# Kernel tuning notes

Measured on AMD Instinct MI355X. Metric: run time of the kernel, lower is better.

The kernel has to match this reference:

```python
import jax, jax.numpy as jnp
import numpy as np
import math

B, L, D = 8, 2048, 256
NUM_TYPES = 1
T_MAX = 200.0
SIGMA = 1.0


def setup_inputs() -> dict:
    key = jax.random.key(0)
    ks = jax.random.split(key, 12)
    event_type = jnp.ones((B, L), dtype=jnp.int64 if jax.config.jax_enable_x64 else jnp.int32)
    t = jax.random.uniform(ks[0], (B, L), dtype=jnp.float32) * T_MAX
    event_time = jnp.sort(t, axis=-1)
    s = 1.0 / math.sqrt(D)
    emb_weight = jax.random.normal(ks[1], (NUM_TYPES + 1, D), jnp.float32)
    emb_weight = emb_weight.at[0].set(0.0)  # padding_idx=0
    gate_w = jax.random.normal(ks[2], (2, D), jnp.float32) * s
    gate_b = jnp.zeros((2,), jnp.float32)
    ker_w = jax.random.normal(ks[3], (1, D), jnp.float32) * s
    ker_b = jnp.zeros((1,), jnp.float32)
    ln_gamma = jnp.ones((D,), jnp.float32)
    ln_beta = jnp.zeros((D,), jnp.float32)
    gen_input_w = jax.random.normal(ks[4], (D, D), jnp.float32) * s
    gen_noise_w = jax.random.normal(ks[5], (D, D), jnp.float32) * s
    gen_out_w = jax.random.normal(ks[6], (1, D), jnp.float32) * s
    gen_out_b = jnp.zeros((1,), jnp.float32)
    noise = jax.random.uniform(ks[7], (B, L, D), jnp.float32)  # torch.rand noise in Generator
    return dict(event_type=event_type, event_time=event_time, emb_weight=emb_weight,
                gate_w=gate_w, gate_b=gate_b, ker_w=ker_w, ker_b=ker_b,
                ln_gamma=ln_gamma, ln_beta=ln_beta, gen_input_w=gen_input_w,
                gen_noise_w=gen_noise_w, gen_out_w=gen_out_w, gen_out_b=gen_out_b,
                noise=noise)


def _softplus_beta(x, beta):
    return jax.nn.softplus(beta * x) / beta


def reference(event_type, event_time, emb_weight, gate_w, gate_b, ker_w, ker_b,
              ln_gamma, ln_beta, gen_input_w, gen_noise_w, gen_out_w, gen_out_b, noise):
    d_model = emb_weight.shape[-1]
    # ---- temporal positional encoding (this is `embedding`) ----
    pos_vec = jnp.power(10000.0, 2.0 * jnp.arange(d_model, dtype=jnp.float32) / d_model)
    t = event_time[:, :, None] / pos_vec                      # [B,L,D]
    idx = jnp.arange(d_model)
    temp_enc = jnp.where(idx % 2 == 0, jnp.sin(t), jnp.cos(t))
    # ---- type embedding ----
    te = emb_weight[event_type] * math.sqrt(d_model)          # [B,L,D]
    # ---- pairwise |t_i - t_j| ; xt[b,i,j]=t_i, xt_bar[b,i,j]=t_j ----
    dt = jnp.abs(event_time[:, :, None] - event_time[:, None, :])  # [B,L,L]
    # ---- squared exponential kernel: params depend only on row i (xd[b,i,j]=te[b,i]) ----
    ls = _softplus_beta(te @ ker_w.T + ker_b, 0.2)[..., 0]    # [B,L]
    scores_k = (SIGMA ** 2) * jnp.exp(-(dt ** 2) / (ls[:, :, None] ** 2))
    # ---- sigmoid gate ----
    p = jax.nn.sigmoid(te @ gate_w.T + gate_b)                # [B,L,2]
    l = p[..., 0][:, :, None]
    s = p[..., 1][:, :, None]
    gate = 1.0 + 0.5 * jnp.tanh((dt / T_MAX - l) / s)
    scores = scores_k * gate                                  # [B,L,L]
    # ---- causal mask: strictly-upper-triangle -> -1e10, then softmax ----
    causal = jnp.tril(jnp.ones((event_time.shape[1], event_time.shape[1]), jnp.bool_))
    scores = jnp.where(causal[None], scores, -1e10)
    attn = jax.nn.softmax(scores, axis=-1)
    # ---- hidden = attn @ temp_enc, layernorm ----
    hidden = jnp.einsum('bij,bjd->bid', attn, temp_enc)
    mu = hidden.mean(-1, keepdims=True)
    var = hidden.var(-1, keepdims=True)
    hidden = (hidden - mu) / jnp.sqrt(var + 1e-6) * ln_gamma + ln_beta
    # ---- Generator (dropout in eval = identity) ----
    h = jax.nn.relu(noise @ gen_noise_w.T + hidden @ gen_input_w.T)
    out = jax.nn.softplus(h @ gen_out_w.T + gen_out_b)[..., 0]  # [B,L]
    return out
```

## Files before the change

### kernel.cpp

```cpp
#include <hip/hip_runtime.h>
#include <hip/hip_bf16.h>

#define BD 8
#define LD 2048
#define DD 256

typedef unsigned short ushort_t;
typedef __attribute__((ext_vector_type(8))) short short8;
typedef __attribute__((ext_vector_type(4))) float floatx4;

__device__ __forceinline__ ushort_t f2bfu(float x) {
  __hip_bfloat16 h = __float2bfloat16(x);
  return *reinterpret_cast<ushort_t*>(&h);
}

__device__ __forceinline__ void dma16(const ushort_t* g, ushort_t* l) {
  __builtin_amdgcn_global_load_lds(
      (const __attribute__((address_space(1))) unsigned int*)g,
      (__attribute__((address_space(3))) unsigned int*)l,
      16, 0, 0);
}

#define WAIT_VM0  0x0F70
#define WAIT_VM8  0x0F78
#define WAIT_VM10 0x0F7A
#define WAIT_LGKM 0xC07F

__device__ __forceinline__ float sin_acc(float a) {
  float k = rintf(a * 0.15915494f);
  float r = __builtin_fmaf(-k, 6.2831855f, a);
  r = __builtin_fmaf(-k, -1.7484555e-7f, r);
  return __sinf(r);
}
__device__ __forceinline__ float cos_acc(float a) {
  float k = rintf(a * 0.15915494f);
  float r = __builtin_fmaf(-k, 6.2831855f, a);
  r = __builtin_fmaf(-k, -1.7484555e-7f, r);
  return __cosf(r);
}

__global__ __launch_bounds__(256) void k_prep(
    const int* __restrict__ etype, const float* __restrict__ etime,
    const float* __restrict__ embw, const float* __restrict__ gatew,
    const float* __restrict__ gateb, const float* __restrict__ kerw,
    const float* __restrict__ kerb, const float* __restrict__ noise,
    const float* __restrict__ wn, const float* __restrict__ wi,
    ushort_t* __restrict__ enc_bf, ushort_t* __restrict__ noise_bf,
    ushort_t* __restrict__ wcat, float* __restrict__ ptable)
{
  const int bk = blockIdx.x;
  const int tid = threadIdx.x;
  if (bk < 4224) {
    int idx = bk * 256 + tid;
    if (idx < 1048576) {
      float4 f = ((const float4*)noise)[idx];
      ushort4 u;
      u.x = f2bfu(f.x); u.y = f2bfu(f.y); u.z = f2bfu(f.z); u.w = f2bfu(f.w);
      *(ushort4*)(noise_bf + (size_t)idx * 4) = u;
    } else {
      int p = idx - 1048576;
      int c = p >> 7;
      int k = (p & 127) * 4;
      const float* src = (k < 256) ? (wn + c * 256 + k) : (wi + c * 256 + (k - 256));
      float4 f = *(const float4*)src;
      ushort4 u;
      u.x = f2bfu(f.x); u.y = f2bfu(f.y); u.z = f2bfu(f.z); u.w = f2bfu(f.w);
      *(ushort4*)(wcat + (((size_t)(c >> 4) * 16 + (k >> 5)) * 512)
                       + (c & 15) * 32 + (k & 31)) = u;
    }
  } else if (bk < 4736) {
    int ebk = bk - 4224;
    __shared__ float ts[32];
    if (tid < 32) ts[tid] = etime[(ebk >> 6) * LD + (ebk & 63) * 32 + tid];
    __syncthreads();
    uint4* dst = (uint4*)(enc_bf + (size_t)ebk * 8192);
    const int jb = (tid & 3) * 8;
    #pragma unroll
    for (int jblk = 0; jblk < 4; ++jblk) {
      int d = jblk * 64 + (tid >> 2);
      float freq = __expf(-0.07195578416f * (float)d);
      unsigned int pk[4];
      #pragma unroll
      for (int p = 0; p < 4; ++p) {
        float a0 = ts[jb + 2 * p] * freq;
        float a1 = ts[jb + 2 * p + 1] * freq;
        float v0 = (d & 1) ? cos_acc(a0) : sin_acc(a0);
        float v1 = (d & 1) ? cos_acc(a1) : sin_acc(a1);
        pk[p] = (unsigned int)f2bfu(v0) | ((unsigned int)f2bfu(v1) << 16);
      }
      dst[jblk * 256 + tid] = make_uint4(pk[0], pk[1], pk[2], pk[3]);
    }
  } else {
    __shared__ float red[4][3];
    int lane = tid & 63, wvi = tid >> 6;
    for (int ty = 0; ty < 2; ++ty) {
      float te = embw[ty * DD + tid] * 16.0f;
      float p1 = te * kerw[tid];
      float p2 = te * gatew[tid];
      float p3 = te * gatew[DD + tid];
      #pragma unroll
      for (int off = 32; off > 0; off >>= 1) {
        p1 += __shfl_xor(p1, off);
        p2 += __shfl_xor(p2, off);
        p3 += __shfl_xor(p3, off);
      }
      if (lane == 0) { red[wvi][0] = p1; red[wvi][1] = p2; red[wvi][2] = p3; }
      __syncthreads();
      if (tid == 0) {
        float s1 = red[0][0] + red[1][0] + red[2][0] + red[3][0] + kerb[0];
        float s2 = red[0][1] + red[1][1] + red[2][1] + red[3][1] + gateb[0];
        float s3 = red[0][2] + red[1][2] + red[2][2] + red[3][2] + gateb[1];
        float z = 0.2f * s1;
        float sp = (z > 15.0f) ? z : log1pf(__expf(z));
        float ls = 5.0f * sp;
        ptable[ty * 4 + 0] = 1.0f / (ls * ls);
        ptable[ty * 4 + 1] = 1.0f / (1.0f + __expf(-s2));
        float s = 1.0f / (1.0f + __expf(-s3));
        ptable[ty * 4 + 2] = 1.0f / s;
      }
      __syncthreads();
    }
  }
}

__global__ __launch_bounds__(128) void k_attn(
    const ushort_t* __restrict__ enc_bf, const float* __restrict__ etime,
    const int* __restrict__ etype, const float* __restrict__ ptable,
    const float* __restrict__ gamma, const float* __restrict__ beta,
    ushort_t* __restrict__ hidden_bf)
{
  __shared__ __align__(16) ushort_t stage[2][2][4096];
  const int tid = threadIdx.x;
  const int lane = tid & 63, wv = tid >> 6;
  const int bk = blockIdx.x;
  const int b = bk & 7;
  const int tl = 127 - (bk >> 3);
  const int base = b * LD;
  const int m = lane & 15, kg = lane >> 4;
  const int i = tl * 16 + m;
  const float ti = etime[base + i];
  const int ty = etype[base + i];
  const float il = ptable[ty * 4 + 0];
  const float ll = ptable[ty * 4 + 1];
  const float is2 = 2.0f * ptable[ty * 4 + 2];
  floatx4 acc[16];
  #pragma unroll
  for (int nt = 0; nt < 16; ++nt) acc[nt] = (floatx4){0.f, 0.f, 0.f, 0.f};
  const int nch = tl / 2 + 1;
  const int myn = (nch > wv) ? ((nch - wv + 1) >> 1) : 0;
  const ushort_t* __restrict__ encC = enc_bf + (size_t)(b * 64) * 8192;
  const int boff = m * 32 + kg * 8;
  ushort_t* bufA = &stage[wv][0][0];
  ushort_t* bufB = &stage[wv][1][0];

  if (myn > 0) {
    const int c0 = wv;
    float4 ta = *(const float4*)(etime + base + c0 * 32 + kg * 8);
    float4 tc = *(const float4*)(etime + base + c0 * 32 + kg * 8 + 4);
    {
      const ushort_t* g = encC + (size_t)c0 * 8192 + lane * 8;
      #pragma unroll
      for (int q = 0; q < 8; ++q) dma16(g + q * 512, bufA + q * 512);
      #pragma unroll
      for (int q = 0; q < 8; ++q) dma16(g + (q + 8) * 512, bufB + q * 512);
    }
    float tj[8] = {ta.x, ta.y, ta.z, ta.w, tc.x, tc.y, tc.z, tc.w};
    short8 af;
    {
      const int j0 = c0 * 32 + kg * 8;
      #pragma unroll
      for (int v = 0; v < 8; ++v) {
        float dt = ti - tj[v];
        float sk = __expf(-dt * dt * il);
        float rg = __builtin_amdgcn_rcpf(__expf((dt * 0.005f - ll) * is2) + 1.0f);
        float w = __expf(sk * (1.5f - rg));
        w = (j0 + v <= i) ? w : 0.0f;
        af[v] = (short)f2bfu(w);
      }
    }
    for (int idx = 0; idx < myn; ++idx) {
      const int ch = wv + 2 * idx;
      const bool more = (idx + 1 < myn);
      const int cn = more ? (ch + 2) : wv;
      __builtin_amdgcn_s_waitcnt(WAIT_VM8);
      #pragma unroll
      for (int q = 0; q < 8; ++q) {
        short8 bf = *(const short8*)(bufA + q * 512 + boff);
        acc[q] = __builtin_amdgcn_mfma_f32_16x16x32_bf16(af, bf, acc[q], 0, 0, 0);
      }
      float4 na = *(const float4*)(etime + base + cn * 32 + kg * 8);
      float4 nc = *(const float4*)(etime + base + cn * 32 + kg * 8 + 4);
      __builtin_amdgcn_s_waitcnt(WAIT_LGKM);
      {
        const ushort_t* g = encC + (size_t)cn * 8192 + lane * 8;
        #pragma unroll
        for (int q = 0; q < 8; ++q) dma16(g + q * 512, bufA + q * 512);
      }
      __builtin_amdgcn_s_waitcnt(WAIT_VM10);
      #pragma unroll
      for (int q = 0; q < 8; ++q) {
        short8 bf = *(const short8*)(bufB + q * 512 + boff);
        acc[8 + q] = __builtin_amdgcn_mfma_f32_16x16x32_bf16(af, bf, acc[8 + q], 0, 0, 0);
      }
      __builtin_amdgcn_s_waitcnt(WAIT_LGKM);
      {
        const ushort_t* g = encC + (size_t)cn * 8192 + lane * 8;
        #pragma unroll
        for (int q = 0; q < 8; ++q) dma16(g + (q + 8) * 512, bufB + q * 512);
      }
      if (more) {
        float ntj[8] = {na.x, na.y, na.z, na.w, nc.x, nc.y, nc.z, nc.w};
        const int j0 = cn * 32 + kg * 8;
        #pragma unroll
        for (int v = 0; v < 8; ++v) {
          float dt = ti - ntj[v];
          float sk = __expf(-dt * dt * il);
          float rg = __builtin_amdgcn_rcpf(__expf((dt * 0.005f - ll) * is2) + 1.0f);
          float w = __expf(sk * (1.5f - rg));
          w = (j0 + v <= i) ? w : 0.0f;
          af[v] = (short)f2bfu(w);
        }
      }
    }
  }
  __syncthreads();
  floatx4* reg = (floatx4*)&stage[0][0][0];
  if (wv == 1) {
    #pragma unroll
    for (int nt = 0; nt < 16; ++nt) reg[nt * 64 + lane] = acc[nt];
  }
  __syncthreads();
  if (wv == 0) {
    #pragma unroll
    for (int nt = 0; nt < 16; ++nt) acc[nt] += reg[nt * 64 + lane];
    float gl[16], cl[16];
    #pragma unroll
    for (int nt = 0; nt < 16; ++nt) { gl[nt] = gamma[nt * 16 + m]; cl[nt] = beta[nt * 16 + m]; }
    const int q = lane >> 4;
    #pragma unroll
    for (int r = 0; r < 4; ++r) {
      float h[16];
      float sm = 0.0f, sq = 0.0f;
      #pragma unroll
      for (int nt = 0; nt < 16; ++nt) {
        h[nt] = acc[nt][r];
        sm += h[nt]; sq += h[nt] * h[nt];
      }
      #pragma unroll
      for (int off = 1; off < 16; off <<= 1) {
        sm += __shfl_xor(sm, off);
        sq += __shfl_xor(sq, off);
      }
      float mean = sm * (1.0f / 256.0f);
      float var = sq * (1.0f / 256.0f) - mean * mean;
      float rstd = rsqrtf(var + 1e-6f);
      const int row = q * 4 + r;
      ushort_t* dst = hidden_bf + ((size_t)(base + tl * 16 + row)) * DD + m;
      #pragma unroll
      for (int nt = 0; nt < 16; ++nt)
        dst[nt * 16] = f2bfu((h[nt] - mean) * rstd * gl[nt] + cl[nt]);
    }
  }
}

__global__ __launch_bounds__(256) void k_gen(
    const ushort_t* __restrict__ noise_bf, const ushort_t* __restrict__ hidden_bf,
    const ushort_t* __restrict__ wcat, const float* __restrict__ wout,
    const float* __restrict__ bout, float* __restrict__ out)
{
  __shared__ float pbuf[4][2][16];
  const int tid = threadIdx.x;
  const int lane = tid & 63, wv = tid >> 6;
  const int m = lane & 15, kg = lane >> 4;
  const int r0 = blockIdx.x * 32 + m;
  const ushort_t* __restrict__ an0 = noise_bf + (size_t)r0 * DD;
  const ushort_t* __restrict__ an1 = noise_bf + (size_t)(r0 + 16) * DD;
  const ushort_t* __restrict__ ah0 = hidden_bf + (size_t)r0 * DD;
  const ushort_t* __restrict__ ah1 = hidden_bf + (size_t)(r0 + 16) * DD;
  floatx4 acc[2][4];
  #pragma unroll
  for (int t = 0; t < 2; ++t)
    #pragma unroll
    for (int n = 0; n < 4; ++n) acc[t][n] = (floatx4){0.f, 0.f, 0.f, 0.f};
  const int slot = m * 32 + kg * 8;
  #pragma unroll
  for (int ks = 0; ks < 16; ++ks) {
    const int koff = (ks & 7) * 32 + kg * 8;
    short8 a0 = *(const short8*)(((ks < 8) ? an0 : ah0) + koff);
    short8 a1 = *(const short8*)(((ks < 8) ? an1 : ah1) + koff);
    #pragma unroll
    for (int n = 0; n < 4; ++n) {
      const ushort_t* bp = wcat + ((size_t)(wv * 4 + n) * 16 + ks) * 512 + slot;
      short8 bf = *(const short8*)bp;
      acc[0][n] = __builtin_amdgcn_mfma_f32_16x16x32_bf16(a0, bf, acc[0][n], 0, 0, 0);
      acc[1][n] = __builtin_amdgcn_mfma_f32_16x16x32_bf16(a1, bf, acc[1][n], 0, 0, 0);
    }
  }
  float wo_l[4];
  #pragma unroll
  for (int n = 0; n < 4; ++n) wo_l[n] = wout[(wv * 4 + n) * 16 + m];
  #pragma unroll
  for (int t = 0; t < 2; ++t) {
    #pragma unroll
    for (int r4 = 0; r4 < 4; ++r4) {
      float p = 0.0f;
      #pragma unroll
      for (int n = 0; n < 4; ++n) p += fmaxf(acc[t][n][r4], 0.0f) * wo_l[n];
      #pragma unroll
      for (int off = 1; off < 16; off <<= 1) p += __shfl_xor(p, off);
      if (m == 0) pbuf[wv][t][kg * 4 + r4] = p;
    }
  }
  __syncthreads();
  if (tid < 32) {
    int t = tid >> 4, rr = tid & 15;
    float x = pbuf[0][t][rr] + pbuf[1][t][rr] + pbuf[2][t][rr] + pbuf[3][t][rr] + bout[0];
    float sp = (x > 15.0f) ? x : log1pf(__expf(x));
    out[blockIdx.x * 32 + t * 16 + rr] = sp;
  }
}

extern "C" void kernel_launch(void* const* d_in, const int* in_sizes, int n_in,
                              void* d_out, int out_size, void* d_ws, size_t ws_size,
                              hipStream_t stream) {
  const int*   etype = (const int*)d_in[0];
  const float* etime = (const float*)d_in[1];
  const float* embw  = (const float*)d_in[2];
  const float* gatew = (const float*)d_in[3];
  const float* gateb = (const float*)d_in[4];
  const float* kerw  = (const float*)d_in[5];
  const float* kerb  = (const float*)d_in[6];
  const float* gamma = (const float*)d_in[7];
  const float* beta  = (const float*)d_in[8];
  const float* wi    = (const float*)d_in[9];
  const float* wn    = (const float*)d_in[10];
  const float* wo    = (const float*)d_in[11];
  const float* bo    = (const float*)d_in[12];
  const float* noise = (const float*)d_in[13];
  float* out = (float*)d_out;

  char* w8 = (char*)d_ws;
  float* ptable       = (float*)(w8);
  ushort_t* enc_bf    = (ushort_t*)(w8 + 262144);
  ushort_t* hidden_bf = (ushort_t*)(w8 + 262144 + 8388608);
  ushort_t* noise_bf  = (ushort_t*)(w8 + 262144 + 2 * 8388608);
  ushort_t* wcat      = (ushort_t*)(w8 + 262144 + 3 * 8388608);

  k_prep<<<4737, 256, 0, stream>>>(etype, etime, embw, gatew, gateb, kerw, kerb,
                                   noise, wn, wi, enc_bf, noise_bf, wcat, ptable);
  k_attn<<<1024, 128, 0, stream>>>(enc_bf, etime, etype, ptable,
                                   gamma, beta, hidden_bf);
  k_gen<<<512, 256, 0, stream>>>(noise_bf, hidden_bf, wcat, wo, bo, out);
}
```

Baseline: 163.5 us.

## Fuse prep, attention and generator into one cooperative persistent kernel

Replaces the three separate launches with one cooperative kernel of 512 blocks that uses grid-wide syncs between the prep, attention and generator phases. Each block pairs a short causal tile with a long one (tl and 127-tl) so every block gets equal work, and both tiles share the same staged encoding chunks. The generator phase reads weights straight from global memory rather than staging them. This removes launch gaps and tail imbalance but adds the cost of grid barriers, heavier register use for two accumulator sets, and only 2 blocks per CU, which may underuse the GPU. The three-kernel path remains as a fallback if the occupancy check or cooperative launch fails.

```diff
diff --git a/kernel.cpp b/kernel.cpp
--- a/kernel.cpp
+++ b/kernel.cpp
@@ -1,7 +1,9 @@
 #include <hip/hip_runtime.h>
 #include <hip/hip_bf16.h>
-
-#define BD 8
+#include <hip/hip_cooperative_groups.h>
+
+namespace cg = cooperative_groups;
+
 #define LD 2048
 #define DD 256
 
@@ -21,10 +23,8 @@
       16, 0, 0);
 }
 
-#define WAIT_VM0  0x0F70
-#define WAIT_VM8  0x0F78
 #define WAIT_VM10 0x0F7A
-#define WAIT_LGKM 0xC07F
+#define WAIT_VM18 0x4F72
 
 __device__ __forceinline__ float sin_acc(float a) {
   float k = rintf(a * 0.15915494f);
@@ -39,7 +39,291 @@
   return __cosf(r);
 }
 
-__global__ __launch_bounds__(256) void k_prep(
+__device__ __forceinline__ short8 make_af(float ti, int i, int j0, const float* tj,
+                                          float il, float ll, float is2) {
+  short8 af;
+  #pragma unroll
+  for (int v = 0; v < 8; ++v) {
+    float dt = ti - tj[v];
+    float sk = __expf(-dt * dt * il);
+    float rg = __builtin_amdgcn_rcpf(__expf((dt * 0.005f - ll) * is2) + 1.0f);
+    float w = __expf(sk * (1.5f - rg));
+    w = (j0 + v <= i) ? w : 0.0f;
+    af[v] = (short)f2bfu(w);
+  }
+  return af;
+}
+
+__global__ __launch_bounds__(128, 2) void k_fused(
+    const int* __restrict__ etype, const float* __restrict__ etime,
+    const float* __restrict__ embw, const float* __restrict__ gatew,
+    const float* __restrict__ gateb, const float* __restrict__ kerw,
+    const float* __restrict__ kerb, const float* __restrict__ gamma,
+    const float* __restrict__ beta, const float* __restrict__ wi,
+    const float* __restrict__ wn, const float* __restrict__ wo,
+    const float* __restrict__ bo, const float* __restrict__ noise,
+    float* __restrict__ out, ushort_t* __restrict__ enc_bf,
+    ushort_t* __restrict__ noise_bf, ushort_t* __restrict__ wcat,
+    float* __restrict__ ptable, ushort_t* __restrict__ hidden_bf)
+{
+  __shared__ __align__(16) ushort_t stage[2][2][8192];
+  const int tid = threadIdx.x;
+  const int lane = tid & 63, wv = tid >> 6;
+  const int bk = blockIdx.x;
+  const int m = lane & 15, kg = lane >> 4;
+  const int qd = lane >> 4;
+  cg::grid_group gg = cg::this_grid();
+
+  {
+    float* ts = (float*)&stage[0][0][0];
+    if (tid < 32) ts[tid] = etime[(bk >> 6) * LD + (bk & 63) * 32 + tid];
+    __syncthreads();
+    uint4* dst = (uint4*)(enc_bf + (size_t)bk * 8192);
+    #pragma unroll
+    for (int it = 0; it < 8; ++it) {
+      int u = it * 128 + tid;
+      int d = u >> 2, jb = (u & 3) * 8;
+      float freq = __expf(-0.07195578416f * (float)d);
+      unsigned int pk[4];
+      #pragma unroll
+      for (int p = 0; p < 4; ++p) {
+        float a0 = ts[jb + 2 * p] * freq;
+        float a1 = ts[jb + 2 * p + 1] * freq;
+        float v0 = (d & 1) ? cos_acc(a0) : sin_acc(a0);
+        float v1 = (d & 1) ? cos_acc(a1) : sin_acc(a1);
+        pk[p] = (unsigned int)f2bfu(v0) | ((unsigned int)f2bfu(v1) << 16);
+      }
+      dst[u] = make_uint4(pk[0], pk[1], pk[2], pk[3]);
+    }
+  }
+  #pragma unroll 1
+  for (int it = 0; it < 17; ++it) {
+    int idx = it * 65536 + bk * 128 + tid;
+    if (idx < 1081344) {
+      if (idx < 1048576) {
+        float4 f = ((const float4*)noise)[idx];
+        ushort4 u;
+        u.x = f2bfu(f.x); u.y = f2bfu(f.y); u.z = f2bfu(f.z); u.w = f2bfu(f.w);
+        *(ushort4*)(noise_bf + (size_t)idx * 4) = u;
+      } else {
+        int p = idx - 1048576;
+        int c = p >> 7;
+        int k = (p & 127) * 4;
+        const float* src = (k < 256) ? (wn + c * 256 + k) : (wi + c * 256 + k - 256);
+        float4 f = *(const float4*)src;
+        ushort4 u;
+        u.x = f2bfu(f.x); u.y = f2bfu(f.y); u.z = f2bfu(f.z); u.w = f2bfu(f.w);
+        *(ushort4*)(wcat + ((size_t)(c >> 4) * 16 + (k >> 5)) * 512
+                         + (c & 15) * 32 + (k & 31)) = u;
+      }
+    }
+  }
+  if (bk == 511) {
+    __syncthreads();
+    float* red = (float*)&stage[0][0][0];
+    for (int ty = 0; ty < 2; ++ty) {
+      float p1 = 0.f, p2 = 0.f, p3 = 0.f;
+      for (int dd = tid; dd < 256; dd += 128) {
+        float te = embw[ty * DD + dd] * 16.0f;
+        p1 += te * kerw[dd];
+        p2 += te * gatew[dd];
+        p3 += te * gatew[DD + dd];
+      }
+      #pragma unroll
+      for (int off = 32; off > 0; off >>= 1) {
+        p1 += __shfl_xor(p1, off);
+        p2 += __shfl_xor(p2, off);
+        p3 += __shfl_xor(p3, off);
+      }
+      if (lane == 0) { red[wv * 3 + 0] = p1; red[wv * 3 + 1] = p2; red[wv * 3 + 2] = p3; }
+      __syncthreads();
+      if (tid == 0) {
+        float s1 = red[0] + red[3] + kerb[0];
+        float s2 = red[1] + red[4] + gateb[0];
+        float s3 = red[2] + red[5] + gateb[1];
+        float z = 0.2f * s1;
+        float sp = (z > 15.0f) ? z : log1pf(__expf(z));
+        float ls = 5.0f * sp;
+        ptable[ty * 4 + 0] = 1.0f / (ls * ls);
+        ptable[ty * 4 + 1] = 1.0f / (1.0f + __expf(-s2));
+        float s = 1.0f / (1.0f + __expf(-s3));
+        ptable[ty * 4 + 2] = 1.0f / s;
+      }
+      __syncthreads();
+    }
+  }
+  __threadfence();
+  gg.sync();
+
+  const int b = bk & 7;
+  const int pr = bk >> 3;
+  const int tlA = pr, tlB = 127 - pr;
+  const int base = b * LD;
+  const int iA = tlA * 16 + m, iB = tlB * 16 + m;
+  const float tiA = etime[base + iA], tiB = etime[base + iB];
+  const int tyA = etype[base + iA], tyB = etype[base + iB];
+  const float ilA = ptable[tyA * 4 + 0], llA = ptable[tyA * 4 + 1];
+  const float isA = 2.0f * ptable[tyA * 4 + 2];
+  const float ilB = ptable[tyB * 4 + 0], llB = ptable[tyB * 4 + 1];
+  const float isB = 2.0f * ptable[tyB * 4 + 2];
+  floatx4 aA[16], aB[16];
+  #pragma unroll
+  for (int q = 0; q < 16; ++q) {
+    aA[q] = (floatx4){0.f, 0.f, 0.f, 0.f};
+    aB[q] = (floatx4){0.f, 0.f, 0.f, 0.f};
+  }
+  const int limA = tlA >> 1;
+  const int nch = (tlB >> 1) + 1;
+  const int myn = (nch - wv + 1) >> 1;
+  const ushort_t* __restrict__ encC = enc_bf + (size_t)(b * 64) * 8192;
+  const int boff = m * 32 + kg * 8;
+  ushort_t* buf0 = &stage[wv][0][0];
+  ushort_t* buf1 = &stage[wv][1][0];
+  short8 afA, afB;
+  int ch = wv;
+  {
+    float4 ta = *(const float4*)(etime + base + ch * 32 + kg * 8);
+    float4 tc = *(const float4*)(etime + base + ch * 32 + kg * 8 + 4);
+    const ushort_t* g = encC + (size_t)ch * 8192 + lane * 8;
+    #pragma unroll
+    for (int q = 0; q < 16; ++q) dma16(g + q * 512, buf0 + q * 512);
+    float tj[8] = {ta.x, ta.y, ta.z, ta.w, tc.x, tc.y, tc.z, tc.w};
+    afB = make_af(tiB, iB, ch * 32 + kg * 8, tj, ilB, llB, isB);
+    if (ch <= limA) afA = make_af(tiA, iA, ch * 32 + kg * 8, tj, ilA, llA, isA);
+  }
+  #pragma unroll 1
+  for (int it = 0; it < myn; ++it) {
+    const bool more = (it + 1 < myn);
+    const int chn = more ? ch + 2 : wv;
+    ushort_t* bcur = (it & 1) ? buf1 : buf0;
+    ushort_t* bnxt = (it & 1) ? buf0 : buf1;
+    float4 na = *(const float4*)(etime + base + chn * 32 + kg * 8);
+    float4 nc = *(const float4*)(etime + base + chn * 32 + kg * 8 + 4);
+    {
+      const ushort_t* g = encC + (size_t)chn * 8192 + lane * 8;
+      #pragma unroll
+      for (int q = 0; q < 16; ++q) dma16(g + q * 512, bnxt + q * 512);
+    }
+    __builtin_amdgcn_s_waitcnt(WAIT_VM18);
+    if (ch <= limA) {
+      #pragma unroll
+      for (int q = 0; q < 16; ++q) {
+        short8 bf = *(const short8*)(bcur + q * 512 + boff);
+        aB[q] = __builtin_amdgcn_mfma_f32_16x16x32_bf16(afB, bf, aB[q], 0, 0, 0);
+        aA[q] = __builtin_amdgcn_mfma_f32_16x16x32_bf16(afA, bf, aA[q], 0, 0, 0);
+      }
+    } else {
+      #pragma unroll
+      for (int q = 0; q < 16; ++q) {
+        short8 bf = *(const short8*)(bcur + q * 512 + boff);
+        aB[q] = __builtin_amdgcn_mfma_f32_16x16x32_bf16(afB, bf, aB[q], 0, 0, 0);
+      }
+    }
+    if (more) {
+      float tj[8] = {na.x, na.y, na.z, na.w, nc.x, nc.y, nc.z, nc.w};
+      afB = make_af(tiB, iB, chn * 32 + kg * 8, tj, ilB, llB, isB);
+      if (chn <= limA) afA = make_af(tiA, iA, chn * 32 + kg * 8, tj, ilA, llA, isA);
+    }
+    ch = chn;
+  }
+  __syncthreads();
+  floatx4* redx = (floatx4*)&stage[0][0][0];
+  if (wv == 1) {
+    #pragma unroll
+    for (int q = 0; q < 16; ++q) redx[q * 64 + lane] = aA[q];
+    #pragma unroll
+    for (int q = 0; q < 16; ++q) redx[(16 + q) * 64 + lane] = aB[q];
+  }
+  __syncthreads();
+  if (wv == 0) {
+    #pragma unroll
+    for (int q = 0; q < 16; ++q) {
+      aA[q] += redx[q * 64 + lane];
+      aB[q] += redx[(16 + q) * 64 + lane];
+    }
+    float gl[16], cl[16];
+    #pragma unroll
+    for (int q = 0; q < 16; ++q) { gl[q] = gamma[q * 16 + m]; cl[q] = beta[q * 16 + m]; }
+    #pragma unroll
+    for (int T = 0; T < 2; ++T) {
+      const int tl = T ? tlB : tlA;
+      #pragma unroll
+      for (int r = 0; r < 4; ++r) {
+        float h[16];
+        float sm = 0.f, sq = 0.f;
+        #pragma unroll
+        for (int q = 0; q < 16; ++q) {
+          h[q] = T ? aB[q][r] : aA[q][r];
+          sm += h[q]; sq += h[q] * h[q];
+        }
+        #pragma unroll
+        for (int off = 1; off < 16; off <<= 1) {
+          sm += __shfl_xor(sm, off);
+          sq += __shfl_xor(sq, off);
+        }
+        float mean = sm * (1.0f / 256.0f);
+        float var = sq * (1.0f / 256.0f) - mean * mean;
+        float rstd = rsqrtf(var + 1e-6f);
+        ushort_t* dst = hidden_bf + (size_t)(base + tl * 16 + qd * 4 + r) * DD + m;
+        #pragma unroll
+        for (int q = 0; q < 16; ++q)
+          dst[q * 16] = f2bfu((h[q] - mean) * rstd * gl[q] + cl[q]);
+      }
+    }
+  }
+  __threadfence();
+  gg.sync();
+
+  #pragma unroll 1
+  for (int u = 0; u < 2; ++u) {
+    const int t = bk * 2 + u;
+    const ushort_t* __restrict__ ar =
+        ((wv == 0) ? noise_bf : hidden_bf) + (size_t)(t * 16 + m) * DD;
+    floatx4 g[16];
+    #pragma unroll
+    for (int nt = 0; nt < 16; ++nt) g[nt] = (floatx4){0.f, 0.f, 0.f, 0.f};
+    #pragma unroll 1
+    for (int ksl = 0; ksl < 8; ++ksl) {
+      const int ksg = wv * 8 + ksl;
+      short8 a = *(const short8*)(ar + ksl * 32 + kg * 8);
+      #pragma unroll
+      for (int nt = 0; nt < 16; ++nt) {
+        short8 bfr = *(const short8*)(wcat + ((size_t)nt * 16 + ksg) * 512 + boff);
+        g[nt] = __builtin_amdgcn_mfma_f32_16x16x32_bf16(a, bfr, g[nt], 0, 0, 0);
+      }
+    }
+    __syncthreads();
+    floatx4* redc = (floatx4*)&stage[0][0][0];
+    if (wv == 1) {
+      #pragma unroll
+      for (int nt = 0; nt < 16; ++nt) redc[nt * 64 + lane] = g[nt];
+    }
+    __syncthreads();
+    if (wv == 0) {
+      #pragma unroll
+      for (int nt = 0; nt < 16; ++nt) g[nt] += redc[nt * 64 + lane];
+      float wo_l[16];
+      #pragma unroll
+      for (int nt = 0; nt < 16; ++nt) wo_l[nt] = wo[nt * 16 + m];
+      const float bo_ = bo[0];
+      #pragma unroll
+      for (int r4 = 0; r4 < 4; ++r4) {
+        float p = 0.f;
+        #pragma unroll
+        for (int nt = 0; nt < 16; ++nt) p += fmaxf(g[nt][r4], 0.f) * wo_l[nt];
+        #pragma unroll
+        for (int off = 1; off < 16; off <<= 1) p += __shfl_xor(p, off);
+        if (m == 0) {
+          float x = p + bo_;
+          out[t * 16 + qd * 4 + r4] = (x > 15.0f) ? x : log1pf(__expf(x));
+        }
+      }
+    }
+    __syncthreads();
+  }
+}
+
+__global__ __launch_bounds__(256) void kf_prep(
     const int* __restrict__ etype, const float* __restrict__ etime,
     const float* __restrict__ embw, const float* __restrict__ gatew,
     const float* __restrict__ gateb, const float* __restrict__ kerw,
@@ -61,11 +345,11 @@
       int p = idx - 1048576;
       int c = p >> 7;
       int k = (p & 127) * 4;
-      const float* src = (k < 256) ? (wn + c * 256 + k) : (wi + c * 256 + (k - 256));
+      const float* src = (k < 256) ? (wn + c * 256 + k) : (wi + c * 256 + k - 256);
       float4 f = *(const float4*)src;
       ushort4 u;
       u.x = f2bfu(f.x); u.y = f2bfu(f.y); u.z = f2bfu(f.z); u.w = f2bfu(f.w);
-      *(ushort4*)(wcat + (((size_t)(c >> 4) * 16 + (k >> 5)) * 512)
+      *(ushort4*)(wcat + ((size_t)(c >> 4) * 16 + (k >> 5)) * 512
                        + (c & 15) * 32 + (k & 31)) = u;
     }
   } else if (bk < 4736) {
@@ -123,7 +407,7 @@
   }
 }
 
-__global__ __launch_bounds__(128) void k_attn(
+__global__ __launch_bounds__(128) void kf_attn(
     const ushort_t* __restrict__ enc_bf, const float* __restrict__ etime,
     const int* __restrict__ etype, const float* __restrict__ ptable,
     const float* __restrict__ gamma, const float* __restrict__ beta,
@@ -150,77 +434,56 @@
   const int myn = (nch > wv) ? ((nch - wv + 1) >> 1) : 0;
   const ushort_t* __restrict__ encC = enc_bf + (size_t)(b * 64) * 8192;
   const int boff = m * 32 + kg * 8;
-  ushort_t* bufA = &stage[wv][0][0];
-  ushort_t* bufB = &stage[wv][1][0];
-
+  ushort_t* buf0 = &stage[wv][0][0];
+  ushort_t* buf1 = &stage[wv][1][0];
   if (myn > 0) {
-    const int c0 = wv;
-    float4 ta = *(const float4*)(etime + base + c0 * 32 + kg * 8);
-    float4 tc = *(const float4*)(etime + base + c0 * 32 + kg * 8 + 4);
+    short8 af;
+    int ch = wv;
     {
-      const ushort_t* g = encC + (size_t)c0 * 8192 + lane * 8;
-      #pragma unroll
-      for (int q = 0; q < 8; ++q) dma16(g + q * 512, bufA + q * 512);
-      #pragma unroll
-      for (int q = 0; q < 8; ++q) dma16(g + (q + 8) * 512, bufB + q * 512);
-    }
-    float tj[8] = {ta.x, ta.y, ta.z, ta.w, tc.x, tc.y, tc.z, tc.w};
-    short8 af;
-    {
-      const int j0 = c0 * 32 + kg * 8;
-      #pragma unroll
-      for (int v = 0; v < 8; ++v) {
-        float dt = ti - tj[v];
-        float sk = __expf(-dt * dt * il);
-        float rg = __builtin_amdgcn_rcpf(__expf((dt * 0.005f - ll) * is2) + 1.0f);
-        float w = __expf(sk * (1.5f - rg));
-        w = (j0 + v <= i) ? w : 0.0f;
-        af[v] = (short)f2bfu(w);
-      }
-    }
-    for (int idx = 0; idx < myn; ++idx) {
-      const int ch = wv + 2 * idx;
-      const bool more = (idx + 1 < myn);
-      const int cn = more ? (ch + 2) : wv;
-      __builtin_amdgcn_s_waitcnt(WAIT_VM8);
+      float4 ta = *(const float4*)(etime + base + ch * 32 + kg * 8);
+      float4 tc = *(const float4*)(etime + base + ch * 32 + kg * 8 + 4);
+      const ushort_t* g = encC + (size_t)ch * 8192 + lane * 8;
+      #pragma unroll
+      for (int q = 0; q < 8; ++q) dma16(g + q * 512, buf0 + q * 512);
+      float tj[8] = {ta.x, ta.y, ta.z, ta.w, tc.x, tc.y, tc.z, tc.w};
+      af = make_af(ti, i, ch * 32 + kg * 8, tj, il, ll, is2);
+      const ushort_t* g2 = g + 8 * 512;
+      #pragma unroll
+      for (int q = 0; q < 8; ++q) dma16(g2 + q * 512, buf1 + q * 512);
+    }
+    #pragma unroll 1
+    for (int it = 0; it < myn; ++it) {
+      const bool more = (it + 1 < myn);
+      const int chn = more ? ch + 2 : wv;
+      float4 na = *(const float4*)(etime + base + chn * 32 + kg * 8);
+      float4 nc = *(const float4*)(etime + base + chn * 32 + kg * 8 + 4);
+      __builtin_amdgcn_s_waitcnt(WAIT_VM10);
       #pragma unroll
       for (int q = 0; q < 8; ++q) {
-        short8 bf = *(const short8*)(bufA + q * 512 + boff);
+        short8 bf = *(const short8*)(buf0 + q * 512 + boff);
         acc[q] = __builtin_amdgcn_mfma_f32_16x16x32_bf16(af, bf, acc[q], 0, 0, 0);
       }
-      float4 na = *(const float4*)(etime + base + cn * 32 + kg * 8);
-      float4 nc = *(const float4*)(etime + base + cn * 32 + kg * 8 + 4);
-      __builtin_amdgcn_s_waitcnt(WAIT_LGKM);
       {
-        const ushort_t* g = encC + (size_t)cn * 8192 + lane * 8;
+        const ushort_t* g = encC + (size_t)chn * 8192 + lane * 8;
         #pragma unroll
-        for (int q = 0; q < 8; ++q) dma16(g + q * 512, bufA + q * 512);
+        for (int q = 0; q < 8; ++q) dma16(g + q * 512, buf0 + q * 512);
       }
       __builtin_amdgcn_s_waitcnt(WAIT_VM10);
       #pragma unroll
       for (int q = 0; q < 8; ++q) {
-        short8 bf = *(const short8*)(bufB + q * 512 + boff);
+        short8 bf = *(const short8*)(buf1 + q * 512 + boff);
         acc[8 + q] = __builtin_amdgcn_mfma_f32_16x16x32_bf16(af, bf, acc[8 + q], 0, 0, 0);
       }
-      __builtin_amdgcn_s_waitcnt(WAIT_LGKM);
       {
-        const ushort_t* g = encC + (size_t)cn * 8192 + lane * 8;
+        const ushort_t* g = encC + (size_t)chn * 8192 + (8 + 0) * 512 + lane * 8;
         #pragma unroll
-        for (int q = 0; q < 8; ++q) dma16(g + (q + 8) * 512, bufB + q * 512);
+        for (int q = 0; q < 8; ++q) dma16(g + q * 512, buf1 + q * 512);
       }
       if (more) {
-        float ntj[8] = {na.x, na.y, na.z, na.w, nc.x, nc.y, nc.z, nc.w};
-        const int j0 = cn * 32 + kg * 8;
-        #pragma unroll
-        for (int v = 0; v < 8; ++v) {
-          float dt = ti - ntj[v];
-          float sk = __expf(-dt * dt * il);
-          float rg = __builtin_amdgcn_rcpf(__expf((dt * 0.005f - ll) * is2) + 1.0f);
-          float w = __expf(sk * (1.5f - rg));
-          w = (j0 + v <= i) ? w : 0.0f;
-          af[v] = (short)f2bfu(w);
-        }
-      }
+        float tj[8] = {na.x, na.y, na.z, na.w, nc.x, nc.y, nc.z, nc.w};
+        af = make_af(ti, i, chn * 32 + kg * 8, tj, il, ll, is2);
+      }
+      ch = chn;
     }
   }
   __syncthreads();
@@ -263,7 +526,7 @@
   }
 }
 
-__global__ __launch_bounds__(256) void k_gen(
+__global__ __launch_bounds__(256) void kf_gen(
     const ushort_t* __restrict__ noise_bf, const ushort_t* __restrict__ hidden_bf,
     const ushort_t* __restrict__ wcat, const float* __restrict__ wout,
     const float* __restrict__ bout, float* __restrict__ out)
@@ -346,9 +609,25 @@
   ushort_t* noise_bf  = (ushort_t*)(w8 + 262144 + 2 * 8388608);
   ushort_t* wcat      = (ushort_t*)(w8 + 262144 + 3 * 8388608);
 
-  k_prep<<<4737, 256, 0, stream>>>(etype, etime, embw, gatew, gateb, kerw, kerb,
-                                   noise, wn, wi, enc_bf, noise_bf, wcat, ptable);
-  k_attn<<<1024, 128, 0, stream>>>(enc_bf, etime, etype, ptable,
-                                   gamma, beta, hidden_bf);
-  k_gen<<<512, 256, 0, stream>>>(noise_bf, hidden_bf, wcat, wo, bo, out);
-}
+  int occ = 0;
+  hipError_t e = hipOccupancyMaxActiveBlocksPerMultiprocessor(&occ, k_fused, 128, 0);
+  bool coop = (e == hipSuccess && occ >= 2);
+  if (coop) {
+    void* args[] = {
+        (void*)&etype, (void*)&etime, (void*)&embw, (void*)&gatew, (void*)&gateb,
+        (void*)&kerw, (void*)&kerb, (void*)&gamma, (void*)&beta, (void*)&wi,
+        (void*)&wn, (void*)&wo, (void*)&bo, (void*)&noise, (void*)&out,
+        (void*)&enc_bf, (void*)&noise_bf, (void*)&wcat, (void*)&ptable,
+        (void*)&hidden_bf};
+    e = hipLaunchCooperativeKernel((const void*)k_fused, dim3(512), dim3(128),
+                                   args, 0, stream);
+    coop = (e == hipSuccess);
+  }
+  if (!coop) {
+    kf_prep<<<4737, 256, 0, stream>>>(etype, etime, embw, gatew, gateb, kerw, kerb,
+                                      noise, wn, wi, enc_bf, noise_bf, wcat, ptable);
+    kf_attn<<<1024, 128, 0, stream>>>(enc_bf, etime, etype, ptable,
+                                      gamma, beta, hidden_bf);
+    kf_gen<<<512, 256, 0, stream>>>(noise_bf, hidden_bf, wcat, wo, bo, out);
+  }
+}
```

Result: no change. 163.6 us (+0.1%).
